# Optimization experiments

Measured on AMD Instinct MI355X. Metric: run time of the kernel, lower is better.

Reference implementation:

```python
import jax, jax.numpy as jnp
import numpy as np

B_, C, N, M, DX = 4, 8, 1024, 1024, 1
POINTS_PER_UNIT = 64


def setup_inputs() -> dict:
    key = jax.random.key(0)
    k1, k2, k3 = jax.random.split(key, 3)
    xz = jax.random.uniform(k1, (M, DX), dtype=jnp.float32)          # grid locations
    z = jax.random.normal(k2, (B_, C, M, M), dtype=jnp.float32)      # grid encoding
    x = jax.random.normal(k3, (B_, N, DX), dtype=jnp.float32)        # target locations
    log_scale = jnp.log(jnp.float32(2.0 / POINTS_PER_UNIT))          # learned scalar
    return {"xz": xz, "z": z, "x": x, "log_scale": log_scale}


def reference(xz, z, x, log_scale):
    # pairwise squared distances: (b, n, m)
    dists2 = jnp.sum((x[:, :, None, :] - xz[None, None, :, :]) ** 2, axis=-1)
    # RBF weights
    weights = jnp.exp(-0.5 * dists2 / jnp.exp(2.0 * log_scale))      # (b, n, m)
    # weighted interpolation of grid encoding: (b, c, n, m)
    z1 = jnp.einsum("bnm,bcmk->bcnk", weights, z)
    # outer product z1 @ z1^T: (b, c, n, n)
    z2 = jnp.einsum("bcnk,bcok->bcno", z1, z1)
    return (xz, z2)
```

## Files before the change

### kernel.cpp

```cpp
#include <hip/hip_runtime.h>
#include <hip/hip_bf16.h>


typedef __attribute__((ext_vector_type(8))) unsigned short u16x8;
typedef __attribute__((ext_vector_type(8))) __bf16 bf16x8;
typedef __attribute__((ext_vector_type(4))) float f32x4;

typedef __attribute__((address_space(1))) void gvoid;
typedef __attribute__((address_space(3))) void svoid;
#define GLDS(g, s) __builtin_amdgcn_global_load_lds((gvoid*)(g), (svoid*)(s), 16, 0, 0)
#define BAR() asm volatile("s_barrier" ::: "memory")

__device__ __forceinline__ unsigned short f2bf(float f) {
  unsigned int u = __builtin_bit_cast(unsigned int, f);
  u += 0x7fffu + ((u >> 16) & 1u);
  return (unsigned short)(u >> 16);
}

__device__ __forceinline__ bf16x8 as_bf16x8(u16x8 v) {
  return __builtin_bit_cast(bf16x8, v);
}

__global__ void weights_kernel(const float* __restrict__ xz, const float* __restrict__ x,
                               const float* __restrict__ ls, unsigned short* __restrict__ W) {
  int bn = blockIdx.x;
  float xv = x[bn];
  float coef = -0.5f * __expf(-2.0f * ls[0]);
  unsigned short* Wrow = W + (size_t)bn * 1024;
  #pragma unroll
  for (int i = 0; i < 4; ++i) {
    int m = threadIdx.x + i * 256;
    float d = xv - xz[m];
    Wrow[m] = f2bf(__expf(coef * d * d));
  }
}

__global__ void transpose_kernel(const float* __restrict__ Z, unsigned short* __restrict__ Zt) {
  __shared__ float tile[64][65];
  int bc = blockIdx.z;
  const float* Zp = Z + ((size_t)bc << 20);
  unsigned short* Ztp = Zt + ((size_t)bc << 20);
  int m0 = blockIdx.x * 64, k0 = blockIdx.y * 64;
  int tx = threadIdx.x & 63, tg = threadIdx.x >> 6;
  #pragma unroll
  for (int i = 0; i < 16; ++i) {
    int ml = tg + i * 4;
    tile[ml][tx] = Zp[(size_t)(m0 + ml) * 1024 + k0 + tx];
  }
  __syncthreads();
  int tx2 = (threadIdx.x & 31) * 2, kg = threadIdx.x >> 5;
  #pragma unroll
  for (int i = 0; i < 8; ++i) {
    int kl = kg + i * 8;
    ushort2 v;
    v.x = f2bf(tile[tx2][kl]);
    v.y = f2bf(tile[tx2 + 1][kl]);
    *(ushort2*)&Ztp[(size_t)(k0 + kl) * 1024 + m0 + tx2] = v;
  }
}

template<bool A_PER_B>
__global__ __launch_bounds__(512, 2)
void gemm_nt8(const unsigned short* __restrict__ A, const unsigned short* __restrict__ B,
              unsigned short* __restrict__ Cbf) {
  extern __shared__ __align__(16) char smem[];

  const int bid = blockIdx.x;
  const int w = ((bid & 7) << 6) + (bid >> 3);
  const int bc = w >> 4;
  const int t  = w & 15;
  const int bi = t & 3, bj = t >> 2;

  const unsigned short* Ap = A + ((size_t)(A_PER_B ? (bc >> 3) : bc) << 20);
  const unsigned short* Bp = B + ((size_t)bc << 20);
  const int tid = threadIdx.x;
  const int wv = tid >> 6, lane = tid & 63;
  const int wr = wv >> 2, wc = wv & 3;
  const int la = lane & 15, ha = lane >> 4;

  f32x4 acc[8][4] = {};

  const int slog = (lane & 7) ^ (lane >> 3);
  const int rloc = 2 * (lane >> 3) + (slog & 1);
  const int cloc = (slog >> 1) * 8;
  const unsigned short* gA0 = Ap + (size_t)(bi*256 +       wv*16 + rloc) * 1024 + cloc;
  const unsigned short* gA1 = Ap + (size_t)(bi*256 + 128 + wv*16 + rloc) * 1024 + cloc;
  const unsigned short* gB0 = Bp + (size_t)(bj*256 +       wv*16 + rloc) * 1024 + cloc;
  const unsigned short* gB1 = Bp + (size_t)(bj*256 + 128 + wv*16 + rloc) * 1024 + cloc;
  const int ldsw = wv * 1024;

  auto stageA = [&](int d, int kh, int kt) {
    const int ko = kt * 64 + kh * 32;
    char* dst = smem + d * 32768 + kh * 16384 + ldsw;
    GLDS(gA0 + ko, dst); GLDS(gA1 + ko, dst + 8192);
  };
  auto stageB = [&](int d, int kh, int kt) {
    const int ko = kt * 64 + kh * 32;
    char* dst = smem + 65536 + d * 32768 + kh * 16384 + ldsw;
    GLDS(gB0 + ko, dst); GLDS(gB1 + ko, dst + 8192);
  };

  const int sphys = ((ha << 1) | (la & 1)) ^ (la >> 1);
  const int abase = wr * 8192 + (la >> 1) * 128 + sphys * 16;
  const int bbase = 65536 + wc * 4096 + (la >> 1) * 128 + sphys * 16;

  u16x8 aX[4], aY[4], b0[4], b1[4];
  auto lda4 = [&](u16x8* dst, int d, int kh, int ms) {
    const char* p = smem + d * 32768 + kh * 16384 + ms * 4096 + abase;
    dst[0] = *(const u16x8*)(p);
    dst[1] = *(const u16x8*)(p + 1024);
    dst[2] = *(const u16x8*)(p + 2048);
    dst[3] = *(const u16x8*)(p + 3072);
  };
  auto ldb4 = [&](u16x8* dst, int d, int kh) {
    const char* p = smem + d * 32768 + kh * 16384 + bbase;
    dst[0] = *(const u16x8*)(p);
    dst[1] = *(const u16x8*)(p + 1024);
    dst[2] = *(const u16x8*)(p + 2048);
    dst[3] = *(const u16x8*)(p + 3072);
  };
  auto mfma16 = [&](const u16x8* Af, const u16x8* Bf, int ms) {
    __builtin_amdgcn_s_setprio(1);
    #pragma unroll
    for (int i = 0; i < 4; ++i)
      #pragma unroll
      for (int n = 0; n < 4; ++n)
        acc[ms * 4 + i][n] = __builtin_amdgcn_mfma_f32_16x16x32_bf16(
            as_bf16x8(Af[i]), as_bf16x8(Bf[n]), acc[ms * 4 + i][n], 0, 0, 0);
    __builtin_amdgcn_s_setprio(0);
  };

  stageA(0, 0, 0); stageB(0, 0, 0);
  stageA(0, 1, 0); stageB(0, 1, 0);
  stageA(1, 0, 1); stageB(1, 0, 1);
  asm volatile("s_waitcnt vmcnt(8)" ::: "memory");
  BAR();
  ldb4(b0, 0, 0); lda4(aX, 0, 0, 0);

  for (int tt = 0; tt < 14; ++tt) {
    const int d = tt & 1;
    stageA(d ^ 1, 1, tt + 1);
    lda4(aY, d, 0, 1);
    mfma16(aX, b0, 0);
    stageB(d ^ 1, 1, tt + 1);
    asm volatile("s_waitcnt vmcnt(8)" ::: "memory");
    BAR();
    ldb4(b1, d, 1); lda4(aX, d, 1, 0);
    mfma16(aY, b0, 1);
    stageA(d, 0, tt + 2);
    lda4(aY, d, 1, 1);
    mfma16(aX, b1, 0);
    stageB(d, 0, tt + 2);
    asm volatile("s_waitcnt vmcnt(8)" ::: "memory");
    BAR();
    ldb4(b0, d ^ 1, 0); lda4(aX, d ^ 1, 0, 0);
    mfma16(aY, b1, 1);
  }
  stageA(1, 1, 15);
  lda4(aY, 0, 0, 1);
  mfma16(aX, b0, 0);
  stageB(1, 1, 15);
  asm volatile("s_waitcnt vmcnt(8)" ::: "memory");
  BAR();
  ldb4(b1, 0, 1); lda4(aX, 0, 1, 0);
  mfma16(aY, b0, 1);
  lda4(aY, 0, 1, 1);
  mfma16(aX, b1, 0);
  asm volatile("s_waitcnt vmcnt(4)" ::: "memory");
  BAR();
  ldb4(b0, 1, 0); lda4(aX, 1, 0, 0);
  mfma16(aY, b1, 1);
  lda4(aY, 1, 0, 1);
  mfma16(aX, b0, 0);
  asm volatile("s_waitcnt vmcnt(0)" ::: "memory");
  BAR();
  ldb4(b1, 1, 1); lda4(aX, 1, 1, 0);
  mfma16(aY, b0, 1);
  lda4(aY, 1, 1, 1);
  mfma16(aX, b1, 0);
  mfma16(aY, b1, 1);
  BAR();

  const size_t cb20 = (size_t)bc << 20;
  unsigned short* sE = (unsigned short*)(smem) + wv * 1152;
  const int r2 = lane >> 2, ch = lane & 3;
  #pragma unroll
  for (int mb = 0; mb < 8; ++mb) {
    #pragma unroll
    for (int nb = 0; nb < 4; ++nb)
      #pragma unroll
      for (int j = 0; j < 4; ++j)
        sE[(ha * 4 + j) * 72 + nb * 16 + la] = f2bf(acc[mb][nb][j]);
    u16x8 v0 = *(const u16x8*)&sE[r2 * 72 + ch * 16];
    u16x8 v1 = *(const u16x8*)&sE[r2 * 72 + ch * 16 + 8];
    unsigned short* gp = Cbf + cb20 +
        (size_t)(bi * 256 + wr * 128 + mb * 16 + r2) * 1024 + bj * 256 + wc * 64 + ch * 16;
    *(u16x8*)gp = v0;
    *(u16x8*)(gp + 8) = v1;
  }
}

__global__ __launch_bounds__(256, 3)
void gemm2_sym(const unsigned short* __restrict__ A, float* __restrict__ Cf) {
  __shared__ __align__(16) char smem[49152];

  const int chunk = 144;
  int w = ((int)blockIdx.x & 7) * chunk + ((int)blockIdx.x >> 3);
  int bc = w / 36;
  int t  = w % 36;
  int bi = 0;
  while (t >= 8 - bi) { t -= 8 - bi; ++bi; }
  int bj = bi + t;

  const unsigned short* Ap = A + ((size_t)bc << 20);
  const int tid = threadIdx.x;
  const int wave = tid >> 6, lane = tid & 63;
  const int wr = wave >> 1, wc = wave & 1;
  const int la = lane & 15, ha = lane >> 4;
  f32x4 acc[4][4] = {};

  const int slog = (lane & 7) ^ ((lane >> 3) & 7);
  const int rloc = 2 * (lane >> 3) + (slog & 1);
  const int cloc = (slog >> 1) * 8;
  const unsigned short* gA0 = Ap + (size_t)(bi * 128 + (wave * 2)     * 16 + rloc) * 1024 + cloc;
  const unsigned short* gA1 = Ap + (size_t)(bi * 128 + (wave * 2 + 1) * 16 + rloc) * 1024 + cloc;
  const unsigned short* gB0 = Ap + (size_t)(bj * 128 + (wave * 2)     * 16 + rloc) * 1024 + cloc;
  const unsigned short* gB1 = Ap + (size_t)(bj * 128 + (wave * 2 + 1) * 16 + rloc) * 1024 + cloc;

  auto stage = [&](int slot, int kt) {
    char* dA = smem + slot * 8192 + wave * 2048;
    char* dB = smem + 24576 + slot * 8192 + wave * 2048;
    GLDS(gA0 + kt, dA); GLDS(gA1 + kt, dA + 1024);
    GLDS(gB0 + kt, dB); GLDS(gB1 + kt, dB + 1024);
  };

  const int sphys = ((ha << 1) | (la & 1)) ^ (la >> 1);
  const int aoff = wr * 4096 + (la >> 1) * 128 + sphys * 16;
  const int boff = 24576 + wc * 4096 + (la >> 1) * 128 + sphys * 16;

  u16x8 aX[4], bX[4], aY[4], bY[4];
  auto rd = [&](u16x8* da, u16x8* db, int slot) {
    const char* pa = smem + slot * 8192 + aoff;
    const char* pb = smem + slot * 8192 + boff;
    da[0] = *(const u16x8*)(pa);
    da[1] = *(const u16x8*)(pa + 1024);
    da[2] = *(const u16x8*)(pa + 2048);
    da[3] = *(const u16x8*)(pa + 3072);
    db[0] = *(const u16x8*)(pb);
    db[1] = *(const u16x8*)(pb + 1024);
    db[2] = *(const u16x8*)(pb + 2048);
    db[3] = *(const u16x8*)(pb + 3072);
  };
  auto mfma16 = [&](const u16x8* Af, const u16x8* Bf) {
    __builtin_amdgcn_s_setprio(1);
    #pragma unroll
    for (int m = 0; m < 4; ++m)
      #pragma unroll
      for (int n = 0; n < 4; ++n)
        acc[m][n] = __builtin_amdgcn_mfma_f32_16x16x32_bf16(
            as_bf16x8(Af[m]), as_bf16x8(Bf[n]), acc[m][n], 0, 0, 0);
    __builtin_amdgcn_s_setprio(0);
  };

  stage(0, 0); stage(1, 32); stage(2, 64);
  asm volatile("s_waitcnt vmcnt(4)" ::: "memory");
  BAR();
  rd(aX, bX, 0);
  asm volatile("s_waitcnt lgkmcnt(0)" ::: "memory");
  BAR();

  int p0 = 0, p1 = 1, p2 = 2;
  for (int t2 = 0; t2 < 28; t2 += 2) {
    stage(p0, (t2 + 3) * 32);
    rd(aY, bY, p1);
    mfma16(aX, bX);
    asm volatile("s_waitcnt vmcnt(4)" ::: "memory");
    BAR();
    stage(p1, (t2 + 4) * 32);
    rd(aX, bX, p2);
    mfma16(aY, bY);
    asm volatile("s_waitcnt vmcnt(4)" ::: "memory");
    BAR();
    int tmp = p2; p2 = p1; p1 = p0; p0 = tmp;
  }
  stage(p0, 31 * 32);
  rd(aY, bY, p1);
  mfma16(aX, bX);
  asm volatile("s_waitcnt vmcnt(4)" ::: "memory");
  BAR();
  rd(aX, bX, p2);
  mfma16(aY, bY);
  asm volatile("s_waitcnt vmcnt(0)" ::: "memory");
  BAR();
  rd(aY, bY, p0);
  mfma16(aX, bX);
  mfma16(aY, bY);
  BAR();

  const size_t cb20 = (size_t)bc << 20;

  #pragma unroll
  for (int m = 0; m < 4; ++m) {
    int row0 = bi * 128 + wr * 64 + m * 16 + ha * 4;
    #pragma unroll
    for (int n = 0; n < 4; ++n) {
      int col = bj * 128 + wc * 64 + n * 16 + la;
      #pragma unroll
      for (int j = 0; j < 4; ++j)
        Cf[cb20 + (size_t)(row0 + j) * 1024 + col] = acc[m][n][j];
    }
  }
  if (bi != bj) {
    float (*sT)[129] = (float(*)[129])smem;
    #pragma unroll
    for (int b = 0; b < 4; ++b) {
      if (wr == (b >> 1)) {
        #pragma unroll
        for (int dm = 0; dm < 2; ++dm) {
          int m = (b & 1) * 2 + dm;
          #pragma unroll
          for (int n = 0; n < 4; ++n)
            #pragma unroll
            for (int j = 0; j < 4; ++j)
              sT[dm * 16 + ha * 4 + j][wc * 64 + n * 16 + la] = acc[m][n][j];
        }
      }
      __syncthreads();
      int c  = tid >> 1;
      int r0 = (tid & 1) * 16;
      float* gp = Cf + cb20 + (size_t)(bj * 128 + c) * 1024 + bi * 128 + b * 32 + r0;
      #pragma unroll
      for (int q = 0; q < 4; ++q) {
        f32x4 v;
        #pragma unroll
        for (int k = 0; k < 4; ++k) v[k] = sT[r0 + q * 4 + k][c];
        *(f32x4*)(gp + q * 4) = v;
      }
      __syncthreads();
    }
  }
}

extern "C" void kernel_launch(void* const* d_in, const int* in_sizes, int n_in,
                              void* d_out, int out_size, void* d_ws, size_t ws_size,
                              hipStream_t stream) {
  const float* xz = (const float*)d_in[0];
  const float* z  = (const float*)d_in[1];
  const float* x  = (const float*)d_in[2];
  const float* ls = (const float*)d_in[3];
  float* out = (float*)d_out;

  unsigned short* W  = (unsigned short*)d_ws;
  unsigned short* Zt = W + ((size_t)4 << 20);
  unsigned short* z1 = Zt + ((size_t)32 << 20);

  hipFuncSetAttribute((const void*)gemm_nt8<true>,
                      hipFuncAttributeMaxDynamicSharedMemorySize, 131072);

  hipMemcpyAsync(out, xz, 1024 * sizeof(float), hipMemcpyDeviceToDevice, stream);
  weights_kernel<<<4096, 256, 0, stream>>>(xz, x, ls, W);
  transpose_kernel<<<dim3(16, 16, 32), 256, 0, stream>>>(z, Zt);
  gemm_nt8<true><<<512, 512, 131072, stream>>>(W, Zt, z1);
  gemm2_sym<<<32 * 36, 256, 0, stream>>>(z1, out + 1024);
}
```

Baseline: 171.7 us.

## Enlarge symmetric z1·z1ᵀ GEMM tiles to 128x256 and coalesce output stores

```diff
diff --git a/kernel.cpp b/kernel.cpp
--- a/kernel.cpp
+++ b/kernel.cpp
@@ -200,70 +200,72 @@
   }
 }
 
-__global__ __launch_bounds__(256, 3)
+__global__ __launch_bounds__(256, 2)
 void gemm2_sym(const unsigned short* __restrict__ A, float* __restrict__ Cf) {
-  __shared__ __align__(16) char smem[49152];
-
-  const int chunk = 144;
+  extern __shared__ __align__(16) char smem[];
+
+  const int chunk = 80;
   int w = ((int)blockIdx.x & 7) * chunk + ((int)blockIdx.x >> 3);
-  int bc = w / 36;
-  int t  = w % 36;
-  int bi = 0;
-  while (t >= 8 - bi) { t -= 8 - bi; ++bi; }
-  int bj = bi + t;
+  const int bc = w / 20;
+  int t = w % 20;
+  int bi, bj;
+  if (t < 2)       { bj = 0; bi = t; }
+  else if (t < 6)  { bj = 1; bi = t - 2; }
+  else if (t < 12) { bj = 2; bi = t - 6; }
+  else             { bj = 3; bi = t - 12; }
 
   const unsigned short* Ap = A + ((size_t)bc << 20);
   const int tid = threadIdx.x;
-  const int wave = tid >> 6, lane = tid & 63;
-  const int wr = wave >> 1, wc = wave & 1;
+  const int wv = tid >> 6, lane = tid & 63;
   const int la = lane & 15, ha = lane >> 4;
-  f32x4 acc[4][4] = {};
-
-  const int slog = (lane & 7) ^ ((lane >> 3) & 7);
+  f32x4 acc[8][4] = {};
+
+  const int slog = (lane & 7) ^ (lane >> 3);
   const int rloc = 2 * (lane >> 3) + (slog & 1);
   const int cloc = (slog >> 1) * 8;
-  const unsigned short* gA0 = Ap + (size_t)(bi * 128 + (wave * 2)     * 16 + rloc) * 1024 + cloc;
-  const unsigned short* gA1 = Ap + (size_t)(bi * 128 + (wave * 2 + 1) * 16 + rloc) * 1024 + cloc;
-  const unsigned short* gB0 = Ap + (size_t)(bj * 128 + (wave * 2)     * 16 + rloc) * 1024 + cloc;
-  const unsigned short* gB1 = Ap + (size_t)(bj * 128 + (wave * 2 + 1) * 16 + rloc) * 1024 + cloc;
+  const unsigned short* gA0 = Ap + (size_t)(bi*128 + (wv     )*16 + rloc)*1024 + cloc;
+  const unsigned short* gA1 = Ap + (size_t)(bi*128 + (wv +  4)*16 + rloc)*1024 + cloc;
+  const unsigned short* gBq0 = Ap + (size_t)(bj*256 + (wv     )*16 + rloc)*1024 + cloc;
+  const unsigned short* gBq1 = Ap + (size_t)(bj*256 + (wv +  4)*16 + rloc)*1024 + cloc;
+  const unsigned short* gBq2 = Ap + (size_t)(bj*256 + (wv +  8)*16 + rloc)*1024 + cloc;
+  const unsigned short* gBq3 = Ap + (size_t)(bj*256 + (wv + 12)*16 + rloc)*1024 + cloc;
+  const int ldsw = wv * 1024;
 
   auto stage = [&](int slot, int kt) {
-    char* dA = smem + slot * 8192 + wave * 2048;
-    char* dB = smem + 24576 + slot * 8192 + wave * 2048;
-    GLDS(gA0 + kt, dA); GLDS(gA1 + kt, dA + 1024);
-    GLDS(gB0 + kt, dB); GLDS(gB1 + kt, dB + 1024);
+    char* base = smem + slot * 24576;
+    GLDS(gA0 + kt, base + ldsw);
+    GLDS(gA1 + kt, base + 4096 + ldsw);
+    GLDS(gBq0 + kt, base + 8192  + ldsw);
+    GLDS(gBq1 + kt, base + 12288 + ldsw);
+    GLDS(gBq2 + kt, base + 16384 + ldsw);
+    GLDS(gBq3 + kt, base + 20480 + ldsw);
   };
 
   const int sphys = ((ha << 1) | (la & 1)) ^ (la >> 1);
-  const int aoff = wr * 4096 + (la >> 1) * 128 + sphys * 16;
-  const int boff = 24576 + wc * 4096 + (la >> 1) * 128 + sphys * 16;
-
-  u16x8 aX[4], bX[4], aY[4], bY[4];
+  const int roff = (la >> 1) * 128 + sphys * 16;
+
+  u16x8 aX[8], bX[4], aY[8], bY[4];
   auto rd = [&](u16x8* da, u16x8* db, int slot) {
-    const char* pa = smem + slot * 8192 + aoff;
-    const char* pb = smem + slot * 8192 + boff;
-    da[0] = *(const u16x8*)(pa);
-    da[1] = *(const u16x8*)(pa + 1024);
-    da[2] = *(const u16x8*)(pa + 2048);
-    da[3] = *(const u16x8*)(pa + 3072);
-    db[0] = *(const u16x8*)(pb);
-    db[1] = *(const u16x8*)(pb + 1024);
-    db[2] = *(const u16x8*)(pb + 2048);
-    db[3] = *(const u16x8*)(pb + 3072);
-  };
-  auto mfma16 = [&](const u16x8* Af, const u16x8* Bf) {
+    const char* pa = smem + slot * 24576 + roff;
+    #pragma unroll
+    for (int mb = 0; mb < 8; ++mb) da[mb] = *(const u16x8*)(pa + mb * 1024);
+    const char* pb = pa + 8192 + wv * 4096;
+    #pragma unroll
+    for (int nb = 0; nb < 4; ++nb) db[nb] = *(const u16x8*)(pb + nb * 1024);
+  };
+  auto mfma32 = [&](const u16x8* Af, const u16x8* Bf) {
     __builtin_amdgcn_s_setprio(1);
     #pragma unroll
-    for (int m = 0; m < 4; ++m)
-      #pragma unroll
-      for (int n = 0; n < 4; ++n)
-        acc[m][n] = __builtin_amdgcn_mfma_f32_16x16x32_bf16(
-            as_bf16x8(Af[m]), as_bf16x8(Bf[n]), acc[m][n], 0, 0, 0);
+    for (int mb = 0; mb < 8; ++mb)
+      #pragma unroll
+      for (int nb = 0; nb < 4; ++nb)
+        acc[mb][nb] = __builtin_amdgcn_mfma_f32_16x16x32_bf16(
+            as_bf16x8(Af[mb]), as_bf16x8(Bf[nb]), acc[mb][nb], 0, 0, 0);
     __builtin_amdgcn_s_setprio(0);
   };
 
   stage(0, 0); stage(1, 32); stage(2, 64);
-  asm volatile("s_waitcnt vmcnt(4)" ::: "memory");
+  asm volatile("s_waitcnt vmcnt(6)" ::: "memory");
   BAR();
   rd(aX, bX, 0);
   asm volatile("s_waitcnt lgkmcnt(0)" ::: "memory");
@@ -273,70 +275,76 @@
   for (int t2 = 0; t2 < 28; t2 += 2) {
     stage(p0, (t2 + 3) * 32);
     rd(aY, bY, p1);
-    mfma16(aX, bX);
-    asm volatile("s_waitcnt vmcnt(4)" ::: "memory");
+    mfma32(aX, bX);
+    asm volatile("s_waitcnt vmcnt(6)" ::: "memory");
     BAR();
     stage(p1, (t2 + 4) * 32);
     rd(aX, bX, p2);
-    mfma16(aY, bY);
-    asm volatile("s_waitcnt vmcnt(4)" ::: "memory");
+    mfma32(aY, bY);
+    asm volatile("s_waitcnt vmcnt(6)" ::: "memory");
     BAR();
     int tmp = p2; p2 = p1; p1 = p0; p0 = tmp;
   }
   stage(p0, 31 * 32);
   rd(aY, bY, p1);
-  mfma16(aX, bX);
-  asm volatile("s_waitcnt vmcnt(4)" ::: "memory");
+  mfma32(aX, bX);
+  asm volatile("s_waitcnt vmcnt(6)" ::: "memory");
   BAR();
   rd(aX, bX, p2);
-  mfma16(aY, bY);
+  mfma32(aY, bY);
   asm volatile("s_waitcnt vmcnt(0)" ::: "memory");
   BAR();
   rd(aY, bY, p0);
-  mfma16(aX, bX);
-  mfma16(aY, bY);
+  mfma32(aX, bX);
+  mfma32(aY, bY);
   BAR();
 
   const size_t cb20 = (size_t)bc << 20;
 
-  #pragma unroll
-  for (int m = 0; m < 4; ++m) {
-    int row0 = bi * 128 + wr * 64 + m * 16 + ha * 4;
-    #pragma unroll
-    for (int n = 0; n < 4; ++n) {
-      int col = bj * 128 + wc * 64 + n * 16 + la;
-      #pragma unroll
-      for (int j = 0; j < 4; ++j)
-        Cf[cb20 + (size_t)(row0 + j) * 1024 + col] = acc[m][n][j];
+  {
+    float* sF = (float*)(smem + wv * 5120);
+    const int rr = lane >> 2, cch = (lane & 3) * 16;
+    #pragma unroll
+    for (int mb = 0; mb < 8; ++mb) {
+      #pragma unroll
+      for (int nb = 0; nb < 4; ++nb)
+        #pragma unroll
+        for (int j = 0; j < 4; ++j)
+          sF[(ha * 4 + j) * 68 + nb * 16 + la] = acc[mb][nb][j];
+      float* gp = Cf + cb20 +
+          (size_t)(bi * 128 + mb * 16 + rr) * 1024 + bj * 256 + wv * 64 + cch;
+      #pragma unroll
+      for (int q = 0; q < 4; ++q)
+        *(f32x4*)(gp + q * 4) = *(const f32x4*)&sF[rr * 68 + cch + q * 4];
     }
   }
-  if (bi != bj) {
-    float (*sT)[129] = (float(*)[129])smem;
-    #pragma unroll
-    for (int b = 0; b < 4; ++b) {
-      if (wr == (b >> 1)) {
+  BAR();
+
+  float (*sT)[129] = (float(*)[129])smem;
+  #pragma unroll
+  for (int h = 0; h < 2; ++h) {
+    if (2 * bj + h >= 2 * (bi >> 1) + 2) {
+      #pragma unroll
+      for (int b = 0; b < 4; ++b) {
+        if (wv == 2 * h + (b >> 1)) {
+          const int nb0 = (b & 1) * 2;
+          #pragma unroll
+          for (int nn = 0; nn < 2; ++nn)
+            #pragma unroll
+            for (int mb = 0; mb < 8; ++mb)
+              #pragma unroll
+              for (int j = 0; j < 4; ++j)
+                sT[nn * 16 + la][mb * 16 + ha * 4 + j] = acc[mb][nb0 + nn][j];
+        }
+        __syncthreads();
+        const int sr = tid >> 3, cc = (tid & 7) * 16;
+        float* gp = Cf + cb20 +
+            (size_t)((2 * bj + h) * 128 + b * 32 + sr) * 1024 + bi * 128 + cc;
         #pragma unroll
-        for (int dm = 0; dm < 2; ++dm) {
-          int m = (b & 1) * 2 + dm;
-          #pragma unroll
-          for (int n = 0; n < 4; ++n)
-            #pragma unroll
-            for (int j = 0; j < 4; ++j)
-              sT[dm * 16 + ha * 4 + j][wc * 64 + n * 16 + la] = acc[m][n][j];
-        }
+        for (int q = 0; q < 4; ++q)
+          *(f32x4*)(gp + q * 4) = *(const f32x4*)&sT[sr][cc + q * 4];
+        __syncthreads();
       }
-      __syncthreads();
-      int c  = tid >> 1;
-      int r0 = (tid & 1) * 16;
-      float* gp = Cf + cb20 + (size_t)(bj * 128 + c) * 1024 + bi * 128 + b * 32 + r0;
-      #pragma unroll
-      for (int q = 0; q < 4; ++q) {
-        f32x4 v;
-        #pragma unroll
-        for (int k = 0; k < 4; ++k) v[k] = sT[r0 + q * 4 + k][c];
-        *(f32x4*)(gp + q * 4) = v;
-      }
-      __syncthreads();
     }
   }
 }
@@ -356,10 +364,12 @@
 
   hipFuncSetAttribute((const void*)gemm_nt8<true>,
                       hipFuncAttributeMaxDynamicSharedMemorySize, 131072);
+  hipFuncSetAttribute((const void*)gemm2_sym,
+                      hipFuncAttributeMaxDynamicSharedMemorySize, 73728);
 
   hipMemcpyAsync(out, xz, 1024 * sizeof(float), hipMemcpyDeviceToDevice, stream);
   weights_kernel<<<4096, 256, 0, stream>>>(xz, x, ls, W);
   transpose_kernel<<<dim3(16, 16, 32), 256, 0, stream>>>(z, Zt);
   gemm_nt8<true><<<512, 512, 131072, stream>>>(W, Zt, z1);
-  gemm2_sym<<<32 * 36, 256, 0, stream>>>(z1, out + 1024);
-}
+  gemm2_sym<<<640, 256, 73728, stream>>>(z1, out + 1024);
+}
```

Result: slower. 199.5 us (+16.2%).
